# Performance work log

Measured on AMD Instinct MI355X. Metric: run time of the kernel, lower is better.

Reference implementation:

```python
import jax, jax.numpy as jnp
import numpy as np

B, S, DM, H = 4, 1024, 1024, 16
D = DM // H  # attn_head_size = 64


def setup_inputs() -> dict:
    key = jax.random.key(0)
    ks = jax.random.split(key, 16)
    sc = 0.02
    return {
        "hidden_states": jax.random.normal(ks[0], (B, S, DM), jnp.float32),
        "wq": jax.random.normal(ks[1], (DM, DM), jnp.float32) * sc,
        "bq": jax.random.normal(ks[2], (DM,), jnp.float32) * sc,
        "wk": jax.random.normal(ks[3], (DM, DM), jnp.float32) * sc,
        "bk": jax.random.normal(ks[4], (DM,), jnp.float32) * sc,
        "wv": jax.random.normal(ks[5], (DM, DM), jnp.float32) * sc,
        "bv": jax.random.normal(ks[6], (DM,), jnp.float32) * sc,
        "wo": jax.random.normal(ks[7], (DM, DM), jnp.float32) * sc,
        "bo": jax.random.normal(ks[8], (DM,), jnp.float32) * sc,
        "wfq": jax.random.normal(ks[9], (DM, DM), jnp.float32) * sc,
        "bfq": jax.random.normal(ks[10], (DM,), jnp.float32) * sc,
        "wfg": jax.random.normal(ks[11], (DM, DM), jnp.float32) * sc,
        "bfg": jax.random.normal(ks[12], (DM,), jnp.float32) * sc,
        "up": jax.random.normal(ks[13], (H, 1, D), jnp.float32) * sc,
        "uz": jax.random.normal(ks[14], (H, 1, D), jnp.float32) * sc,
    }


def _split_heads(x):
    # [B, S, DM] -> [B, H, S, D]
    return x.reshape(x.shape[0], x.shape[1], H, D).transpose(0, 2, 1, 3)


def reference(hidden_states, wq, bq, wk, bk, wv, bv, wo, bo,
              wfq, bfq, wfg, bfg, up, uz):
    key_len = hidden_states.shape[1]
    mixed_q = hidden_states @ wq + bq  # [B, S, DM]
    mixed_k = hidden_states @ wk + bk
    mixed_v = hidden_states @ wv + bv

    # focus-attention Gaussian bias
    glo = jnp.mean(mixed_q, axis=1, keepdims=True)                      # [B, 1, DM]
    c = jnp.tanh((mixed_q @ wfq + bfq) + (glo @ wfg + bfg))             # [B, S, DM]
    c = _split_heads(c)                                                 # [B, H, S, D]
    p = jnp.sum(c * up[None], axis=-1)                                  # [B, H, S]
    z = jnp.sum(c * uz[None], axis=-1)                                  # [B, H, S]
    P = jax.nn.sigmoid(p) * key_len                                     # [B, H, S]
    Z = jax.nn.sigmoid(z) * key_len
    j = jnp.arange(key_len, dtype=P.dtype)                              # [S]
    # G[b,h,q,k] = -(k - P[b,h,q])^2 * 2 / Z[b,h,q]^2
    G = -((j[None, None, None, :] - P[..., None]) ** 2) * 2.0 / (Z[..., None] ** 2)

    q = _split_heads(mixed_q)
    k = _split_heads(mixed_k)
    v = _split_heads(mixed_v)

    scores = jnp.einsum("bhqd,bhkd->bhqk", q, k) / jnp.sqrt(jnp.float32(D))
    scores = scores + G
    probs = jax.nn.softmax(scores, axis=-1)  # dropout_prob = 0 -> no-op
    ctx = jnp.einsum("bhqk,bhkd->bhqd", probs, v)
    ctx = ctx.transpose(0, 2, 1, 3).reshape(ctx.shape[0], key_len, H * D)
    return ctx @ wo + bo
```

## Files before the change

### kernel.cpp

```cpp
#include <hip/hip_runtime.h>
#include <hip/hip_bf16.h>
#include <stdint.h>

#define DEV __device__ __forceinline__

typedef __attribute__((ext_vector_type(4))) float f32x4;
typedef __attribute__((ext_vector_type(8))) __bf16 bf16x8;
typedef __attribute__((ext_vector_type(4))) __bf16 bf16x4;
typedef __attribute__((ext_vector_type(4))) unsigned int uint4v;
typedef __attribute__((ext_vector_type(4))) int i32x4;

static constexpr int Bc = 4, Sc = 1024, DMc = 1024, Hc = 16, Dh = 64;
static constexpr int Mc = Bc * Sc;

DEV __bf16 f2b(float x) {
    unsigned u = __builtin_bit_cast(unsigned, x);
    unsigned r = (u + 0x7fffu + ((u >> 16) & 1u)) >> 16;
    return __builtin_bit_cast(__bf16, (unsigned short)r);
}
DEV float b2f(__bf16 x) {
    unsigned short s = __builtin_bit_cast(unsigned short, x);
    unsigned u = ((unsigned)s) << 16;
    return __builtin_bit_cast(float, u);
}
DEV unsigned cvt_pk_bf16(float a, float b) {
    unsigned r;
    asm("v_cvt_pk_bf16_f32 %0, %1, %2" : "=v"(r) : "v"(a), "v"(b));
    return r;
}
DEV void gload_lds16(const void* g, void* l) {
    __builtin_amdgcn_global_load_lds(
        (const __attribute__((address_space(1))) unsigned int*)g,
        (__attribute__((address_space(3))) unsigned int*)l,
        16, 0, 0);
}
template <int N> DEV void wvm();
template <> DEV void wvm<0>() { asm volatile("s_waitcnt vmcnt(0)" ::: "memory"); }
template <> DEV void wvm<3>() { asm volatile("s_waitcnt vmcnt(3)" ::: "memory"); }
template <> DEV void wvm<4>() { asm volatile("s_waitcnt vmcnt(4)" ::: "memory"); }
template <> DEV void wvm<6>() { asm volatile("s_waitcnt vmcnt(6)" ::: "memory"); }
template <> DEV void wvm<8>() { asm volatile("s_waitcnt vmcnt(8)" ::: "memory"); }

DEV bf16x8 ldswz32(const __bf16* base, int row, int lg) {
    const char* p = (const char*)base + row * 64 + (((lg) ^ ((row >> 1) & 3)) << 4);
    return *(const bf16x8*)p;
}

__global__ void k_cvt2(const float* __restrict__ hs, __bf16* __restrict__ hsb,
                       float* __restrict__ part0) {
    int sc = blockIdx.x, b = blockIdx.y, tid = threadIdx.x;
    int c0 = tid * 4;
    float4 s = {0.f, 0.f, 0.f, 0.f};
#pragma unroll
    for (int r = 0; r < 8; r++) {
        size_t row = (size_t)b * 1024 + sc * 8 + r;
        float4 v = *(const float4*)&hs[row * 1024 + c0];
        s.x += v.x; s.y += v.y; s.z += v.z; s.w += v.w;
        bf16x4 o = { f2b(v.x), f2b(v.y), f2b(v.z), f2b(v.w) };
        *(bf16x4*)&hsb[row * 1024 + c0] = o;
    }
    *(float4*)&part0[(size_t)(sc * 4 + b) * 1024 + c0] = s;
}

__global__ void k_tcvt5(const float* __restrict__ s0, const float* __restrict__ s1,
                        const float* __restrict__ s2, const float* __restrict__ s3,
                        const float* __restrict__ s4,
                        __bf16* __restrict__ d0, __bf16* __restrict__ d1,
                        __bf16* __restrict__ d2, __bf16* __restrict__ d3,
                        __bf16* __restrict__ d4, __bf16* __restrict__ wqb) {
    __shared__ float t[32][33];
    const float* in; __bf16* out;
    switch (blockIdx.z) {
        case 0: in = s0; out = d0; break;
        case 1: in = s1; out = d1; break;
        case 2: in = s2; out = d2; break;
        case 3: in = s3; out = d3; break;
        default: in = s4; out = d4; break;
    }
    int c0 = blockIdx.x * 32, r0 = blockIdx.y * 32;
    for (int j = 0; j < 4; j++) {
        float v = in[(size_t)(r0 + threadIdx.y + j * 8) * 1024 + c0 + threadIdx.x];
        t[threadIdx.y + j * 8][threadIdx.x] = v;
        if (blockIdx.z == 0)
            wqb[(size_t)(r0 + threadIdx.y + j * 8) * 1024 + c0 + threadIdx.x] = f2b(v);
    }
    __syncthreads();
    for (int j = 0; j < 4; j++)
        out[(size_t)(c0 + threadIdx.y + j * 8) * 1024 + r0 + threadIdx.x] = f2b(t[threadIdx.x][threadIdx.y + j * 8]);
}

template <int EPI, int BM>
__global__ __launch_bounds__(256) void k_gemm(
    const __bf16* __restrict__ A, const __bf16* __restrict__ Bt,
    const float* __restrict__ bias, void* __restrict__ Cout, int N, int K)
{
    constexpr int MF = BM / 32;
    constexpr int ACH = BM / 64;
    __shared__ __bf16 Al[4][BM * 32];
    __shared__ __bf16 Bl[4][128 * 32];
    const int bm = blockIdx.x, bn = blockIdx.y;
    const int tid = threadIdx.x, lane = tid & 63, wid = tid >> 6;
    const int l15 = lane & 15, lg = lane >> 4;
    const int qr = (wid >> 1) * (BM / 2), qc = (wid & 1) * 64;
    f32x4 acc[MF][4] = {};

    const __bf16* Ab = A + (size_t)bm * BM * K;
    const __bf16* Bb = Bt + (size_t)bn * 128 * K;

#define STAGE_G(k0, Ad, Bd)                                                       \
    _Pragma("unroll")                                                             \
    for (int c = 0; c < ACH; c++) {                                               \
        int ch = c * 256 + tid, row = ch >> 2, u = ch & 3;                        \
        int su = u ^ ((row >> 1) & 3);                                            \
        gload_lds16(&Ab[(size_t)row * K + (k0) + su * 8], (Ad) + ch * 8);         \
    }                                                                             \
    _Pragma("unroll")                                                             \
    for (int c = 0; c < 2; c++) {                                                 \
        int ch = c * 256 + tid, row = ch >> 2, u = ch & 3;                        \
        int su = u ^ ((row >> 1) & 3);                                            \
        gload_lds16(&Bb[(size_t)row * K + (k0) + su * 8], (Bd) + ch * 8);         \
    }

    const int T = K / 32;
    STAGE_G(0, &Al[0][0], &Bl[0][0]);
    STAGE_G(32, &Al[1][0], &Bl[1][0]);
    STAGE_G(64, &Al[2][0], &Bl[2][0]);
    wvm<2 * (ACH + 2)>();
    __builtin_amdgcn_s_barrier();

    for (int t = 0; t < T; t++) {
        if (t + 3 < T) { STAGE_G((t + 3) * 32, &Al[(t + 3) & 3][0], &Bl[(t + 3) & 3][0]); }
        const __bf16* Ar = &Al[t & 3][0];
        const __bf16* Br = &Bl[t & 3][0];
        bf16x8 af[MF], bfv[4];
#pragma unroll
        for (int m = 0; m < MF; m++) af[m] = ldswz32(Ar, qr + m * 16 + l15, lg);
#pragma unroll
        for (int n = 0; n < 4; n++) bfv[n] = ldswz32(Br, qc + n * 16 + l15, lg);
#pragma unroll
        for (int m = 0; m < MF; m++)
#pragma unroll
            for (int n = 0; n < 4; n++)
                acc[m][n] = __builtin_amdgcn_mfma_f32_16x16x32_bf16(af[m], bfv[n], acc[m][n], 0, 0, 0);
        if (t + 3 < T) wvm<2 * (ACH + 2)>();
        else if (t + 2 < T) wvm<ACH + 2>();
        else wvm<0>();
        __builtin_amdgcn_s_barrier();
    }
#undef STAGE_G
#pragma unroll
    for (int m = 0; m < MF; m++) {
        int row_base = bm * BM + qr + m * 16 + lg * 4;
#pragma unroll
        for (int n = 0; n < 4; n++) {
            int col = bn * 128 + qc + n * 16 + l15;
            float bsum = bias ? bias[col] : 0.0f;
#pragma unroll
            for (int r = 0; r < 4; r++) {
                int row = row_base + r;
                float v = acc[m][n][r] + bsum;
                if constexpr (EPI == 2) ((float*)Cout)[(size_t)row * N + col] = v;
                else ((__bf16*)Cout)[(size_t)row * N + col] = f2b(v);
            }
        }
    }
}

__global__ __launch_bounds__(256) void k_qkvc(
    const __bf16* __restrict__ A, const __bf16* __restrict__ BtAll,
    const float* __restrict__ bq, const float* __restrict__ bk, const float* __restrict__ bv,
    const float* __restrict__ gt2, const float* __restrict__ up, const float* __restrict__ uz,
    __bf16* __restrict__ mq, __bf16* __restrict__ mk_, __bf16* __restrict__ vt,
    float* __restrict__ Pf, float* __restrict__ Zf)
{
    constexpr int K = 1024;
    __shared__ __bf16 Al[4][128 * 32];
    __shared__ __bf16 Bl[4][128 * 32];
    const int bm = blockIdx.x, bn = blockIdx.y;
    const int tid = threadIdx.x, lane = tid & 63, wid = tid >> 6;
    const int l15 = lane & 15, lg = lane >> 4;
    const int qr = (wid >> 1) * 64, qc = (wid & 1) * 64;
    f32x4 acc[4][4] = {};

    const __bf16* Ab = A + (size_t)bm * 128 * K;
    const __bf16* Bb = BtAll + (size_t)bn * 128 * K;

#define STAGE_Q(k0, Ad, Bd)                                                       \
    _Pragma("unroll")                                                             \
    for (int c = 0; c < 2; c++) {                                                 \
        int ch = c * 256 + tid, row = ch >> 2, u = ch & 3;                        \
        int su = u ^ ((row >> 1) & 3);                                            \
        gload_lds16(&Ab[(size_t)row * K + (k0) + su * 8], (Ad) + ch * 8);         \
        gload_lds16(&Bb[(size_t)row * K + (k0) + su * 8], (Bd) + ch * 8);         \
    }

    STAGE_Q(0, &Al[0][0], &Bl[0][0]);
    STAGE_Q(32, &Al[1][0], &Bl[1][0]);
    STAGE_Q(64, &Al[2][0], &Bl[2][0]);
    wvm<8>();
    __builtin_amdgcn_s_barrier();

    for (int t = 0; t < 32; t++) {
        if (t + 3 < 32) { STAGE_Q((t + 3) * 32, &Al[(t + 3) & 3][0], &Bl[(t + 3) & 3][0]); }
        const __bf16* Ar = &Al[t & 3][0];
        const __bf16* Br = &Bl[t & 3][0];
        bf16x8 af[4], bfv[4];
#pragma unroll
        for (int m = 0; m < 4; m++) af[m] = ldswz32(Ar, qr + m * 16 + l15, lg);
#pragma unroll
        for (int n = 0; n < 4; n++) bfv[n] = ldswz32(Br, qc + n * 16 + l15, lg);
#pragma unroll
        for (int m = 0; m < 4; m++)
#pragma unroll
            for (int n = 0; n < 4; n++)
                acc[m][n] = __builtin_amdgcn_mfma_f32_16x16x32_bf16(af[m], bfv[n], acc[m][n], 0, 0, 0);
        if (t + 3 < 32) wvm<8>();
        else if (t + 2 < 32) wvm<4>();
        else wvm<0>();
        __builtin_amdgcn_s_barrier();
    }
#undef STAGE_Q

    const int chunk = bn >> 3;
    if (chunk == 3) {
        const int h = (bn & 7) * 2 + (qc >> 6);
        float upv[4], uzv[4];
#pragma unroll
        for (int n = 0; n < 4; n++) {
            upv[n] = up[h * 64 + n * 16 + l15];
            uzv[n] = uz[h * 64 + n * 16 + l15];
        }
#pragma unroll
        for (int m = 0; m < 4; m++) {
            int row_base = bm * 128 + qr + m * 16 + lg * 4;
#pragma unroll
            for (int r = 0; r < 4; r++) {
                int row = row_base + r;
                float p = 0.f, z = 0.f;
#pragma unroll
                for (int n = 0; n < 4; n++) {
                    int col = (bn & 7) * 128 + qc + n * 16 + l15;
                    float cv = tanhf(acc[m][n][r] + gt2[(row >> 10) * 1024 + col]);
                    p += cv * upv[n];
                    z += cv * uzv[n];
                }
#pragma unroll
                for (int d = 1; d < 16; d <<= 1) {
                    p += __shfl_xor(p, d, 16);
                    z += __shfl_xor(z, d, 16);
                }
                if (l15 == 0) {
                    int bb = row >> 10, s = row & 1023;
                    Pf[((size_t)(bb * 16 + h)) * 1024 + s] = 1024.f / (1.f + __expf(-p));
                    Zf[((size_t)(bb * 16 + h)) * 1024 + s] = 1024.f / (1.f + __expf(-z));
                }
            }
        }
    } else if (chunk == 2) {
        const int b = bm >> 3;
#pragma unroll
        for (int m = 0; m < 4; m++) {
            int s0 = (bm & 7) * 128 + qr + m * 16 + lg * 4;
#pragma unroll
            for (int n = 0; n < 4; n++) {
                int col = (bn & 7) * 128 + qc + n * 16 + l15;
                int h = col >> 6, d = col & 63;
                float bsum = bv[col];
                bf16x4 o = { f2b(acc[m][n][0] + bsum), f2b(acc[m][n][1] + bsum),
                             f2b(acc[m][n][2] + bsum), f2b(acc[m][n][3] + bsum) };
                *(bf16x4*)&vt[((size_t)((b * 16 + h) * 64 + d)) * 1024 + s0] = o;
            }
        }
    } else {
        const float* bias = chunk == 0 ? bq : bk;
        __bf16* outp = chunk == 0 ? mq : mk_;
#pragma unroll
        for (int m = 0; m < 4; m++) {
            int row_base = bm * 128 + qr + m * 16 + lg * 4;
#pragma unroll
            for (int n = 0; n < 4; n++) {
                int col = (bn & 7) * 128 + qc + n * 16 + l15;
                float bsum = bias[col];
#pragma unroll
                for (int r = 0; r < 4; r++) {
                    int row = row_base + r;
                    outp[(size_t)row * 1024 + col] = f2b(acc[m][n][r] + bsum);
                }
            }
        }
    }
}

__global__ void k_glo2(const float* __restrict__ part0, const float* __restrict__ wq,
                       float* __restrict__ glo_part) {
    __shared__ float ghs_l[256];
    int tid = threadIdx.x, kc = blockIdx.y;
    {
        int bb = tid >> 6, kk = tid & 63, k = kc * 64 + kk;
        float s = 0.f;
        for (int sc = 0; sc < 128; sc++) s += part0[(size_t)(sc * 4 + bb) * 1024 + k];
        ghs_l[tid] = s * (1.0f / 1024.f);
    }
    __syncthreads();
    int n = blockIdx.x * 256 + tid;
    float a0 = 0, a1 = 0, a2 = 0, a3 = 0;
    for (int j = 0; j < 64; j++) {
        float w = wq[(size_t)(kc * 64 + j) * 1024 + n];
        a0 += ghs_l[j] * w; a1 += ghs_l[64 + j] * w; a2 += ghs_l[128 + j] * w; a3 += ghs_l[192 + j] * w;
    }
    glo_part[(kc * 4 + 0) * 1024 + n] = a0;
    glo_part[(kc * 4 + 1) * 1024 + n] = a1;
    glo_part[(kc * 4 + 2) * 1024 + n] = a2;
    glo_part[(kc * 4 + 3) * 1024 + n] = a3;
}
__global__ void k_gt2p(const float* __restrict__ glo_part, const float* __restrict__ bq,
                       const float* __restrict__ wfg, const float* __restrict__ wfq,
                       float* __restrict__ gt_part) {
    __shared__ float glo_l[256];
    int tid = threadIdx.x, kc = blockIdx.y;
    {
        int bb = tid >> 6, kk = tid & 63, k = kc * 64 + kk;
        float s = bq[k];
        for (int k2 = 0; k2 < 16; k2++) s += glo_part[(k2 * 4 + bb) * 1024 + k];
        glo_l[tid] = s;
    }
    __syncthreads();
    int n = blockIdx.x * 256 + tid;
    float a0 = 0, a1 = 0, a2 = 0, a3 = 0, t = 0;
    for (int j = 0; j < 64; j++) {
        int k = kc * 64 + j;
        float wg = wfg[(size_t)k * 1024 + n];
        float wf = wfq[(size_t)k * 1024 + n];
        a0 += glo_l[j] * wg; a1 += glo_l[64 + j] * wg; a2 += glo_l[128 + j] * wg; a3 += glo_l[192 + j] * wg;
        t += bq[k] * wf;
    }
    gt_part[(kc * 4 + 0) * 1024 + n] = a0 + t;
    gt_part[(kc * 4 + 1) * 1024 + n] = a1 + t;
    gt_part[(kc * 4 + 2) * 1024 + n] = a2 + t;
    gt_part[(kc * 4 + 3) * 1024 + n] = a3 + t;
}
__global__ void k_red_gt(const float* __restrict__ gt_part, const float* __restrict__ bfg,
                         const float* __restrict__ bfq, float* __restrict__ gt2) {
    int i = blockIdx.x * 256 + threadIdx.x;
    int b = i >> 10, n = i & 1023;
    float s = bfg[n] + bfq[n];
    for (int kc = 0; kc < 16; kc++) s += gt_part[(kc * 4 + b) * 1024 + n];
    gt2[i] = s;
}

DEV bf16x8 ldfrag(const __bf16* base, int row, int colbyte) {
    const char* p = (const char*)base + (size_t)row * 128 + (colbyte ^ ((row & 7) << 4));
    return *(const bf16x8*)p;
}

__global__ __launch_bounds__(256) void k_attn(
    const __bf16* __restrict__ Q, const __bf16* __restrict__ Kx, const __bf16* __restrict__ Vt_g,
    const float* __restrict__ Pf, const float* __restrict__ Zf, __bf16* __restrict__ ctx)
{
    __shared__ __bf16 Kl[2][64 * 64];
    __shared__ __bf16 Vl[2][64 * 64];
    const int qt = blockIdx.x, h = blockIdx.y, b = blockIdx.z;
    const int tid = threadIdx.x, lane = tid & 63, wid = tid >> 6;
    const int l15 = lane & 15, lg = lane >> 4;
    const int qbase = qt * 128 + wid * 32;
    const size_t qoff = ((size_t)(b * Sc)) * DMc + h * Dh;

    bf16x8 qf[2][2];
#pragma unroll
    for (int qh = 0; qh < 2; qh++)
#pragma unroll
        for (int dh = 0; dh < 2; dh++)
            qf[qh][dh] = *(const bf16x8*)&Q[qoff + (size_t)(qbase + qh * 16 + l15) * DMc + dh * 32 + lg * 8];

    float Pr[2], Ar[2];
#pragma unroll
    for (int qh = 0; qh < 2; qh++) {
        int row = qbase + qh * 16 + l15;
        float pp = Pf[((size_t)(b * 16 + h)) * 1024 + row];
        float zz = Zf[((size_t)(b * 16 + h)) * 1024 + row];
        Pr[qh] = pp; Ar[qh] = 2.0f / (zz * zz);
    }
    float m[2] = {-1e30f, -1e30f}, l[2] = {0.f, 0.f};
    f32x4 oacc[2][4] = {};

    const __bf16* Kbase = Kx + qoff;
    const __bf16* Vbase = Vt_g + ((size_t)((b * 16 + h) * 64)) * 1024;

#pragma unroll
    for (int i = 0; i < 2; i++) {
        int ch = i * 256 + tid, row = ch >> 3, off = ch & 7;
        uint4v kv = *(const uint4v*)&Kbase[(size_t)row * DMc + off * 8];
        uint4v vv = *(const uint4v*)&Vbase[(size_t)row * 1024 + off * 8];
        *(uint4v*)((char*)&Kl[0][0] + row * 128 + ((off * 16) ^ ((row & 7) << 4))) = kv;
        *(uint4v*)((char*)&Vl[0][0] + row * 128 + ((off * 16) ^ ((row & 7) << 4))) = vv;
    }
    __syncthreads();

    for (int t = 0; t < 16; t++) {
        const int buf = t & 1;
        uint4v rk[2], rv[2];
        if (t < 15) {
#pragma unroll
            for (int i = 0; i < 2; i++) {
                int ch = i * 256 + tid, row = ch >> 3, off = ch & 7;
                rk[i] = *(const uint4v*)&Kbase[(size_t)((t + 1) * 64 + row) * DMc + off * 8];
                rv[i] = *(const uint4v*)&Vbase[(size_t)row * 1024 + (t + 1) * 64 + off * 8];
            }
        }

        f32x4 st[2][4];
        __builtin_amdgcn_s_setprio(1);
#pragma unroll
        for (int c = 0; c < 4; c++) {
            bf16x8 kb0 = ldfrag(&Kl[buf][0], c * 16 + l15, lg * 16);
            bf16x8 kb1 = ldfrag(&Kl[buf][0], c * 16 + l15, 64 + lg * 16);
#pragma unroll
            for (int qh = 0; qh < 2; qh++) {
                f32x4 a = {0.f, 0.f, 0.f, 0.f};
                a = __builtin_amdgcn_mfma_f32_16x16x32_bf16(kb0, qf[qh][0], a, 0, 0, 0);
                a = __builtin_amdgcn_mfma_f32_16x16x32_bf16(kb1, qf[qh][1], a, 0, 0, 0);
                st[qh][c] = a;
            }
        }
        __builtin_amdgcn_s_setprio(0);

        int pk[2][4][2];
#pragma unroll
        for (int qh = 0; qh < 2; qh++) {
            float s[16];
            float mx = -1e30f;
#pragma unroll
            for (int c = 0; c < 4; c++)
#pragma unroll
                for (int r = 0; r < 4; r++) {
                    float kidx = (float)(t * 64 + c * 16 + lg * 4 + r);
                    float dk = kidx - Pr[qh];
                    float v = st[qh][c][r] * 0.125f - dk * dk * Ar[qh];
                    s[c * 4 + r] = v;
                    mx = fmaxf(mx, v);
                }
            mx = fmaxf(mx, __shfl_xor(mx, 16, 64));
            mx = fmaxf(mx, __shfl_xor(mx, 32, 64));
            float nm = fmaxf(m[qh], mx);
            float sc_ = __expf(m[qh] - nm);
            m[qh] = nm;
            float rs = 0.f;
#pragma unroll
            for (int i = 0; i < 16; i++) { float p = __expf(s[i] - nm); s[i] = p; rs += p; }
            rs += __shfl_xor(rs, 16, 64);
            rs += __shfl_xor(rs, 32, 64);
            l[qh] = l[qh] * sc_ + rs;
#pragma unroll
            for (int c = 0; c < 4; c++) {
                pk[qh][c][0] = (int)cvt_pk_bf16(s[c * 4 + 0], s[c * 4 + 1]);
                pk[qh][c][1] = (int)cvt_pk_bf16(s[c * 4 + 2], s[c * 4 + 3]);
            }
#pragma unroll
            for (int r = 0; r < 4; r++) {
                float scr = __shfl(sc_, lg * 4 + r, 16);
#pragma unroll
                for (int dt = 0; dt < 4; dt++) oacc[qh][dt][r] *= scr;
            }
        }

        const int a0 = (((lg & 1) << 1) * 16 + l15) * 4;
        const int a1 = a0 + 64;
        const int selhi = lg >> 1;
#pragma unroll
        for (int kh = 0; kh < 2; kh++) {
            bf16x8 vb[4];
#pragma unroll
            for (int dt = 0; dt < 4; dt++) vb[dt] = ldfrag(&Vl[buf][0], dt * 16 + l15, kh * 64 + lg * 16);
#pragma unroll
            for (int qh = 0; qh < 2; qh++) {
                int w[4];
#pragma unroll
                for (int wi = 0; wi < 4; wi++) {
                    int addr = (wi < 2) ? a0 : a1;
                    int pr = wi & 1;
                    int va = __builtin_amdgcn_ds_bpermute(addr, pk[qh][kh * 2 + 0][pr]);
                    int vb2 = __builtin_amdgcn_ds_bpermute(addr, pk[qh][kh * 2 + 1][pr]);
                    w[wi] = selhi ? vb2 : va;
                }
                i32x4 wv = {w[0], w[1], w[2], w[3]};
                bf16x8 pa = __builtin_bit_cast(bf16x8, wv);
                __builtin_amdgcn_s_setprio(1);
#pragma unroll
                for (int dt = 0; dt < 4; dt++)
                    oacc[qh][dt] = __builtin_amdgcn_mfma_f32_16x16x32_bf16(pa, vb[dt], oacc[qh][dt], 0, 0, 0);
                __builtin_amdgcn_s_setprio(0);
            }
        }

        if (t < 15) {
#pragma unroll
            for (int i = 0; i < 2; i++) {
                int ch = i * 256 + tid, row = ch >> 3, off = ch & 7;
                *(uint4v*)((char*)&Kl[buf ^ 1][0] + row * 128 + ((off * 16) ^ ((row & 7) << 4))) = rk[i];
                *(uint4v*)((char*)&Vl[buf ^ 1][0] + row * 128 + ((off * 16) ^ ((row & 7) << 4))) = rv[i];
            }
        }
        __syncthreads();
    }

#pragma unroll
    for (int qh = 0; qh < 2; qh++) {
        float lr[4];
#pragma unroll
        for (int r = 0; r < 4; r++) lr[r] = __shfl(l[qh], lg * 4 + r, 16);
#pragma unroll
        for (int dt = 0; dt < 4; dt++)
#pragma unroll
            for (int r = 0; r < 4; r++) {
                int row = qbase + qh * 16 + lg * 4 + r;
                ctx[((size_t)(b * Sc) + row) * DMc + h * Dh + dt * 16 + l15] =
                    f2b(oacc[qh][dt][r] / lr[r]);
            }
    }
}

extern "C" void kernel_launch(void* const* d_in, const int* in_sizes, int n_in,
                              void* d_out, int out_size, void* d_ws, size_t ws_size,
                              hipStream_t stream) {
    const float* hs  = (const float*)d_in[0];
    const float* wq  = (const float*)d_in[1];
    const float* bq  = (const float*)d_in[2];
    const float* wk  = (const float*)d_in[3];
    const float* bk  = (const float*)d_in[4];
    const float* wv  = (const float*)d_in[5];
    const float* bv  = (const float*)d_in[6];
    const float* wo  = (const float*)d_in[7];
    const float* bo  = (const float*)d_in[8];
    const float* wfq = (const float*)d_in[9];
    const float* bfq = (const float*)d_in[10];
    const float* wfg = (const float*)d_in[11];
    const float* bfg = (const float*)d_in[12];
    const float* up  = (const float*)d_in[13];
    const float* uz  = (const float*)d_in[14];

    char* ws = (char*)d_ws;
    const size_t MB = 1ull << 20;
    __bf16* hsb   = (__bf16*)(ws);
    __bf16* BtAll = (__bf16*)(ws + 8 * MB);
    __bf16* wfqT  = (__bf16*)(ws + 16 * MB);
    __bf16* woT   = (__bf16*)(ws + 18 * MB);
    __bf16* mq    = (__bf16*)(ws + 20 * MB);
    __bf16* mk    = (__bf16*)(ws + 28 * MB);
    __bf16* vt    = (__bf16*)(ws + 36 * MB);
    __bf16* ctxb  = (__bf16*)(ws);
    __bf16* wqb   = (__bf16*)(ws + 55 * MB);
    char* sm = ws + 52 * MB;
    float* Pf       = (float*)(sm);
    float* Zf       = (float*)(sm + (256 << 10));
    float* glo_part = (float*)(sm + (512 << 10));
    float* gt_part  = (float*)(sm + (768 << 10));
    float* gt2      = (float*)(sm + (1024 << 10));
    float* part0    = (float*)(ws + 57 * MB);

    k_cvt2<<<dim3(128, 4), 256, 0, stream>>>(hs, hsb, part0);
    k_tcvt5<<<dim3(32, 32, 5), dim3(32, 8), 0, stream>>>(
        wq, wk, wv, wfq, wo,
        BtAll, BtAll + 1048576, BtAll + 2097152, wfqT, woT, wqb);

    k_glo2<<<dim3(4, 16), 256, 0, stream>>>(part0, wq, glo_part);
    k_gt2p<<<dim3(4, 16), 256, 0, stream>>>(glo_part, bq, wfg, wfq, gt_part);
    k_red_gt<<<16, 256, 0, stream>>>(gt_part, bfg, bfq, gt2);

    k_gemm<0, 64><<<dim3(16, 8), 256, 0, stream>>>(wfqT, wqb, nullptr, BtAll + 3145728, DMc, DMc);

    k_qkvc<<<dim3(32, 32), 256, 0, stream>>>(hsb, BtAll, bq, bk, bv, gt2, up, uz,
                                             mq, mk, vt, Pf, Zf);

    k_attn<<<dim3(8, 16, 4), 256, 0, stream>>>(mq, mk, vt, Pf, Zf, ctxb);

    k_gemm<2, 64><<<dim3(64, 8), 256, 0, stream>>>(ctxb, woT, bo, d_out, DMc, DMc);
}
```

Measured before the change: 190.3 us.

## Enlarge QKVC GEMM tile to 256x256 with 512 threads and triple buffering

The fused QKV/focus GEMM now uses 256x256 output tiles computed by 8 waves of 512 threads, where it used 128x128 tiles with 4 waves. Each wave covers a 128x64 sub-tile with 8x4 MFMA accumulators. The LDS pipeline goes from 4-stage to 3-stage buffering, and the grid shrinks to 16x16 blocks. The larger tile raises arithmetic intensity and reuse of the global loads. The cost is more registers per thread and fewer blocks (256 on a 256-CU part, about one wave of work), and the 2-blocks-per-CU launch bound may not be reachable.

```diff
diff --git a/kernel.cpp b/kernel.cpp
--- a/kernel.cpp
+++ b/kernel.cpp
@@ -166,7 +166,7 @@
     }
 }
 
-__global__ __launch_bounds__(256) void k_qkvc(
+__global__ __launch_bounds__(512, 2) void k_qkvc(
     const __bf16* __restrict__ A, const __bf16* __restrict__ BtAll,
     const float* __restrict__ bq, const float* __restrict__ bk, const float* __restrict__ bv,
     const float* __restrict__ gt2, const float* __restrict__ up, const float* __restrict__ uz,
@@ -174,56 +174,58 @@
     float* __restrict__ Pf, float* __restrict__ Zf)
 {
     constexpr int K = 1024;
-    __shared__ __bf16 Al[4][128 * 32];
-    __shared__ __bf16 Bl[4][128 * 32];
+    __shared__ __bf16 AL[3][2][128 * 32];
+    __shared__ __bf16 BL[3][2][128 * 32];
     const int bm = blockIdx.x, bn = blockIdx.y;
     const int tid = threadIdx.x, lane = tid & 63, wid = tid >> 6;
     const int l15 = lane & 15, lg = lane >> 4;
-    const int qr = (wid >> 1) * 64, qc = (wid & 1) * 64;
-    f32x4 acc[4][4] = {};
-
-    const __bf16* Ab = A + (size_t)bm * 128 * K;
-    const __bf16* Bb = BtAll + (size_t)bn * 128 * K;
-
-#define STAGE_Q(k0, Ad, Bd)                                                       \
-    _Pragma("unroll")                                                             \
-    for (int c = 0; c < 2; c++) {                                                 \
-        int ch = c * 256 + tid, row = ch >> 2, u = ch & 3;                        \
-        int su = u ^ ((row >> 1) & 3);                                            \
-        gload_lds16(&Ab[(size_t)row * K + (k0) + su * 8], (Ad) + ch * 8);         \
-        gload_lds16(&Bb[(size_t)row * K + (k0) + su * 8], (Bd) + ch * 8);         \
-    }
-
-    STAGE_Q(0, &Al[0][0], &Bl[0][0]);
-    STAGE_Q(32, &Al[1][0], &Bl[1][0]);
-    STAGE_Q(64, &Al[2][0], &Bl[2][0]);
-    wvm<8>();
+    const int wr = wid >> 2, wc = wid & 3;
+    const int bhalf = wc >> 1, brow0 = (wc & 1) * 64;
+    f32x4 acc[8][4] = {};
+
+    const __bf16* Ab = A + (size_t)bm * 256 * K;
+    const __bf16* Bb = BtAll + (size_t)bn * 256 * K;
+
+    const int srow = tid >> 2;
+    const int su_ = (tid & 3) ^ ((srow >> 1) & 3);
+
+#define STAGE(k0, buf)                                                                      \
+    gload_lds16(&Ab[(size_t)srow * K + (k0) + su_ * 8],        &AL[buf][0][tid * 8]);       \
+    gload_lds16(&Ab[(size_t)(128 + srow) * K + (k0) + su_ * 8], &AL[buf][1][tid * 8]);      \
+    gload_lds16(&Bb[(size_t)srow * K + (k0) + su_ * 8],        &BL[buf][0][tid * 8]);       \
+    gload_lds16(&Bb[(size_t)(128 + srow) * K + (k0) + su_ * 8], &BL[buf][1][tid * 8]);
+
+    STAGE(0, 0);
+    STAGE(32, 1);
+    wvm<4>();
     __builtin_amdgcn_s_barrier();
 
+    int brd = 0, bst = 2;
     for (int t = 0; t < 32; t++) {
-        if (t + 3 < 32) { STAGE_Q((t + 3) * 32, &Al[(t + 3) & 3][0], &Bl[(t + 3) & 3][0]); }
-        const __bf16* Ar = &Al[t & 3][0];
-        const __bf16* Br = &Bl[t & 3][0];
-        bf16x8 af[4], bfv[4];
-#pragma unroll
-        for (int m = 0; m < 4; m++) af[m] = ldswz32(Ar, qr + m * 16 + l15, lg);
-#pragma unroll
-        for (int n = 0; n < 4; n++) bfv[n] = ldswz32(Br, qc + n * 16 + l15, lg);
-#pragma unroll
-        for (int m = 0; m < 4; m++)
+        if (t + 2 < 32) { STAGE((t + 2) * 32, bst); }
+        const __bf16* Ar = &AL[brd][wr][0];
+        const __bf16* Br = &BL[brd][bhalf][0];
+        bf16x8 bfv[4];
+#pragma unroll
+        for (int n = 0; n < 4; n++) bfv[n] = ldswz32(Br, brow0 + n * 16 + l15, lg);
+#pragma unroll
+        for (int m = 0; m < 8; m++) {
+            bf16x8 af = ldswz32(Ar, m * 16 + l15, lg);
 #pragma unroll
             for (int n = 0; n < 4; n++)
-                acc[m][n] = __builtin_amdgcn_mfma_f32_16x16x32_bf16(af[m], bfv[n], acc[m][n], 0, 0, 0);
-        if (t + 3 < 32) wvm<8>();
-        else if (t + 2 < 32) wvm<4>();
+                acc[m][n] = __builtin_amdgcn_mfma_f32_16x16x32_bf16(af, bfv[n], acc[m][n], 0, 0, 0);
+        }
+        if (t + 2 < 32) wvm<4>();
         else wvm<0>();
         __builtin_amdgcn_s_barrier();
-    }
-#undef STAGE_Q
-
-    const int chunk = bn >> 3;
+        brd = brd == 2 ? 0 : brd + 1;
+        bst = bst == 2 ? 0 : bst + 1;
+    }
+#undef STAGE
+
+    const int chunk = bn >> 2;
     if (chunk == 3) {
-        const int h = (bn & 7) * 2 + (qc >> 6);
+        const int h = (bn & 3) * 4 + wc;
         float upv[4], uzv[4];
 #pragma unroll
         for (int n = 0; n < 4; n++) {
@@ -231,15 +233,15 @@
             uzv[n] = uz[h * 64 + n * 16 + l15];
         }
 #pragma unroll
-        for (int m = 0; m < 4; m++) {
-            int row_base = bm * 128 + qr + m * 16 + lg * 4;
+        for (int m = 0; m < 8; m++) {
+            int row_base = bm * 256 + wr * 128 + m * 16 + lg * 4;
 #pragma unroll
             for (int r = 0; r < 4; r++) {
                 int row = row_base + r;
                 float p = 0.f, z = 0.f;
 #pragma unroll
                 for (int n = 0; n < 4; n++) {
-                    int col = (bn & 7) * 128 + qc + n * 16 + l15;
+                    int col = (bn & 3) * 256 + wc * 64 + n * 16 + l15;
                     float cv = tanhf(acc[m][n][r] + gt2[(row >> 10) * 1024 + col]);
                     p += cv * upv[n];
                     z += cv * uzv[n];
@@ -257,15 +259,15 @@
             }
         }
     } else if (chunk == 2) {
-        const int b = bm >> 3;
-#pragma unroll
-        for (int m = 0; m < 4; m++) {
-            int s0 = (bm & 7) * 128 + qr + m * 16 + lg * 4;
+        const int h = (bn & 3) * 4 + wc;
+#pragma unroll
+        for (int m = 0; m < 8; m++) {
+            int row0 = bm * 256 + wr * 128 + m * 16 + lg * 4;
+            int b = row0 >> 10, s0 = row0 & 1023;
 #pragma unroll
             for (int n = 0; n < 4; n++) {
-                int col = (bn & 7) * 128 + qc + n * 16 + l15;
-                int h = col >> 6, d = col & 63;
-                float bsum = bv[col];
+                int d = n * 16 + l15;
+                float bsum = bv[h * 64 + d];
                 bf16x4 o = { f2b(acc[m][n][0] + bsum), f2b(acc[m][n][1] + bsum),
                              f2b(acc[m][n][2] + bsum), f2b(acc[m][n][3] + bsum) };
                 *(bf16x4*)&vt[((size_t)((b * 16 + h) * 64 + d)) * 1024 + s0] = o;
@@ -275,11 +277,11 @@
         const float* bias = chunk == 0 ? bq : bk;
         __bf16* outp = chunk == 0 ? mq : mk_;
 #pragma unroll
-        for (int m = 0; m < 4; m++) {
-            int row_base = bm * 128 + qr + m * 16 + lg * 4;
+        for (int m = 0; m < 8; m++) {
+            int row_base = bm * 256 + wr * 128 + m * 16 + lg * 4;
 #pragma unroll
             for (int n = 0; n < 4; n++) {
-                int col = (bn & 7) * 128 + qc + n * 16 + l15;
+                int col = (bn & 3) * 256 + wc * 64 + n * 16 + l15;
                 float bsum = bias[col];
 #pragma unroll
                 for (int r = 0; r < 4; r++) {
@@ -568,7 +570,7 @@
 
     k_gemm<0, 64><<<dim3(16, 8), 256, 0, stream>>>(wfqT, wqb, nullptr, BtAll + 3145728, DMc, DMc);
 
-    k_qkvc<<<dim3(32, 32), 256, 0, stream>>>(hsb, BtAll, bq, bk, bv, gt2, up, uz,
+    k_qkvc<<<dim3(16, 16), 512, 0, stream>>>(hsb, BtAll, bq, bk, bv, gt2, up, uz,
                                              mq, mk, vt, Pf, Zf);
 
     k_attn<<<dim3(8, 16, 4), 256, 0, stream>>>(mq, mk, vt, Pf, Zf, ctxb);
```

After: 194.9 us. 2.4% more time.
